# Kernel optimization log

Measured on AMD Instinct MI355X. Metric: run time of the kernel, lower is better.

## Reference

```python
import jax, jax.numpy as jnp
import numpy as np

B, T_CTX, N_EMBD, N_ATTN, N_HEAD = 8, 1024, 1024, 1024, 16
HEAD_SIZE = N_ATTN // N_HEAD


def _init_time_w():
    # replicates the torch init: per-head exponential decay curves
    curve = np.array([-(T_CTX - 1 - i) for i in range(T_CTX)], dtype=np.float64)
    ww = np.ones((N_HEAD, T_CTX), dtype=np.float32)
    for h in range(N_HEAD):
        if h < N_HEAD - 1:
            decay_speed = T_CTX ** (-(h + 1) / (N_HEAD - 1))
        else:
            decay_speed = 0.0
        ww[h] = np.exp(curve * decay_speed).astype(np.float32)
    return jnp.asarray(ww)


def setup_inputs() -> dict:
    key = jax.random.key(0)
    ks = jax.random.split(key, 6)
    s = 0.02
    return {
        "x": jax.random.normal(ks[0], (B, T_CTX, N_EMBD), jnp.float32),
        "time_w": _init_time_w(),                                   # [H, TT]
        "time_alpha": jnp.ones((N_HEAD, 1, T_CTX), jnp.float32),
        "time_beta": jnp.ones((N_HEAD, T_CTX, 1), jnp.float32),
        "time_gamma": jnp.ones((T_CTX, 1), jnp.float32),
        "Wk": jax.random.normal(ks[1], (N_ATTN, N_EMBD), jnp.float32) * s,
        "bk": jnp.zeros((N_ATTN,), jnp.float32),
        "Wv": jax.random.normal(ks[2], (N_ATTN, N_EMBD), jnp.float32) * s,
        "bv": jnp.zeros((N_ATTN,), jnp.float32),
        "Wr": jax.random.normal(ks[3], (N_ATTN, N_EMBD), jnp.float32) * s,
        "br": jnp.zeros((N_ATTN,), jnp.float32),
        "Wo": jax.random.normal(ks[4], (N_EMBD, N_ATTN), jnp.float32) * s,
        "bo": jnp.zeros((N_EMBD,), jnp.float32),
    }


def _build_w(time_w, time_alpha, time_beta, T):
    # w[h,t,u] = time_w[h, TT-1-(t-u)] for u<=t else 0  (causal decay matrix)
    TT = time_w.shape[1]
    t = jnp.arange(T)[:, None]
    u = jnp.arange(T)[None, :]
    idx = jnp.clip((TT - 1) - t + u, 0, TT - 1)
    mask = u <= t
    w = jnp.where(mask[None, :, :], time_w[:, idx], 0.0)  # [H, T, T]
    return w * time_alpha[:, :, :T] * time_beta[:, :T, :]


def reference(x, time_w, time_alpha, time_beta, time_gamma,
              Wk, bk, Wv, bv, Wr, br, Wo, bo):
    Bb, T, C = x.shape
    H = time_w.shape[0]
    w = _build_w(time_w, time_alpha, time_beta, T)  # [H,T,T]

    # time shift on the first half of channels: prepend zero row, drop last
    x_half = jnp.pad(x[:, :, : C // 2], ((0, 0), (1, 0), (0, 0)))[:, :T, :]
    xs = jnp.concatenate([x_half, x[:, :, C // 2 :]], axis=-1)

    k = xs @ Wk.T + bk
    v = xs @ Wv.T + bv
    r = xs @ Wr.T + br

    k = jnp.exp(jnp.clip(k, -60.0, 30.0))
    sum_k = jnp.cumsum(k, axis=1)  # [B,T,NA]

    kv = (k * v).reshape(Bb, T, H, -1)               # [B,T,H,hs]
    wkv = jnp.einsum('htu,buhc->bthc', w, kv).reshape(Bb, T, -1)

    rwkv = jax.nn.sigmoid(r) * wkv / sum_k
    out = rwkv @ Wo.T + bo
    return out * time_gamma[:T]
```

## Files before the change

### kernel.cpp

```cpp
#include <hip/hip_runtime.h>
#include <hip/hip_bf16.h>
#include <cstddef>
#include <cstdint>

#define B_SZ   8
#define T_CTX  1024
#define C_DIM  1024
#define H_NUM  16
#define HS     64
#define M_ROWS (B_SZ * T_CTX)

typedef __attribute__((ext_vector_type(8))) short bf16x8;
typedef __attribute__((ext_vector_type(8))) unsigned short u16x8;
typedef __attribute__((ext_vector_type(4))) float f32x4;

static __device__ inline unsigned short f2bf(float f) {
    __hip_bfloat16 h = __float2bfloat16(f);
    return __builtin_bit_cast(unsigned short, h);
}
static __device__ inline float bf2f(unsigned short u) {
    unsigned int v = ((unsigned int)u) << 16;
    return __builtin_bit_cast(float, v);
}
static __device__ inline void gld16(const void* g, void* l) {
    __builtin_amdgcn_global_load_lds((const __attribute__((address_space(1))) void*)g,
                                     (__attribute__((address_space(3))) void*)l,
                                     16, 0, 0);
}

__global__ __launch_bounds__(256)
void convert_all(const float* __restrict__ x, unsigned short* __restrict__ xs,
                 const float* __restrict__ Wk, const float* __restrict__ Wv,
                 const float* __restrict__ Wr, const float* __restrict__ Wo,
                 unsigned short* __restrict__ wdst)
{
    const int bid = blockIdx.x;
    if (bid < 8192) {
        const int idx = (bid * 256 + threadIdx.x) * 4;
        const int m = idx >> 10;
        const int c = idx & 1023;
        float4 v;
        if (c < 512) {
            const int t = m & (T_CTX - 1);
            if (t == 0) v = make_float4(0.f, 0.f, 0.f, 0.f);
            else        v = *(const float4*)(x + (size_t)(m - 1) * C_DIM + c);
        } else {
            v = *(const float4*)(x + idx);
        }
        ushort4 o;
        o.x = f2bf(v.x); o.y = f2bf(v.y); o.z = f2bf(v.z); o.w = f2bf(v.w);
        *(ushort4*)(xs + idx) = o;
    } else {
        const int wid = bid - 8192;
        const int z = wid >> 10;
        const float* src = (z == 0) ? Wk : (z == 1) ? Wv : (z == 2) ? Wr : Wo;
        const int idx = ((wid & 1023) * 256 + threadIdx.x) * 4;
        const float4 v = *(const float4*)(src + idx);
        ushort4 o;
        o.x = f2bf(v.x); o.y = f2bf(v.y); o.z = f2bf(v.z); o.w = f2bf(v.w);
        *(ushort4*)(wdst + (size_t)z * (C_DIM * C_DIM) + idx) = o;
    }
}

__global__ __launch_bounds__(256, 2)
void mfma_gemm64(const unsigned short* __restrict__ A,
                 const unsigned short* __restrict__ Wb,
                 const float* __restrict__ b0, const float* __restrict__ b1,
                 const float* __restrict__ b2,
                 void* __restrict__ o0, void* __restrict__ o1, void* __restrict__ o2,
                 const float* __restrict__ gamma, int multi)
{
    const int d  = blockIdx.x;
    const int y  = ((d & 7) << 3) | ((d >> 3) & 7);
    const int xb = d >> 6;
    const int m0 = y * 128, n0 = xb * 128;

    int mode, ncol0;
    const float* bias;
    void* out;
    if (multi) {
        const int z = n0 >> 10;
        mode = z;
        ncol0 = n0 & 1023;
        bias = (z == 0) ? b0 : (z == 1) ? b1 : b2;
        out  = (z == 0) ? o0 : (z == 1) ? o1 : o2;
    } else {
        mode = 3; ncol0 = n0; bias = b0; out = o0;
    }

    __shared__ unsigned short Sh[2 * 128 * 64];

    const int tid = threadIdx.x;
    const int w = tid >> 6, l = tid & 63;

    const int r8  = l >> 3;
    const int c16 = ((l & 7) ^ r8) * 8;
    const unsigned short* gA = A  + (size_t)(m0 + w * 32 + r8) * C_DIM + c16;
    const unsigned short* gB = Wb + (size_t)(n0 + w * 32 + r8) * C_DIM + c16;
    char* lA = (char*)Sh + (w * 32) * 128;
    char* lB = (char*)Sh + 16384 + (w * 32) * 128;

    const int wr = w >> 1, wc = w & 1;
    const int lr = l & 15, lkq = l >> 4;
    const int x7 = lr & 7;

    f32x4 acc[4][4];
    #pragma unroll
    for (int i = 0; i < 4; ++i)
        #pragma unroll
        for (int j = 0; j < 4; ++j) acc[i][j] = (f32x4){0.f, 0.f, 0.f, 0.f};

    for (int k0 = 0; k0 < C_DIM; k0 += 64) {
        #pragma unroll
        for (int r = 0; r < 4; ++r) {
            gld16(gA + k0 + (size_t)r * 8 * C_DIM, lA + r * 8 * 128);
            gld16(gB + k0 + (size_t)r * 8 * C_DIM, lB + r * 8 * 128);
        }
        __syncthreads();

        bf16x8 af[2][4], bfv[2][4];
        #pragma unroll
        for (int ks = 0; ks < 2; ++ks) {
            const int slot = ((ks * 4 + lkq) ^ x7) * 8;
            #pragma unroll
            for (int i = 0; i < 4; ++i)
                af[ks][i] = *(const bf16x8*)&Sh[(wr * 64 + i * 16 + lr) * 64 + slot];
            #pragma unroll
            for (int j = 0; j < 4; ++j)
                bfv[ks][j] = *(const bf16x8*)&Sh[8192 + (wc * 64 + j * 16 + lr) * 64 + slot];
        }
        #pragma unroll
        for (int ks = 0; ks < 2; ++ks)
            #pragma unroll
            for (int i = 0; i < 4; ++i)
                #pragma unroll
                for (int j = 0; j < 4; ++j)
                    acc[i][j] = __builtin_amdgcn_mfma_f32_16x16x32_bf16(
                        af[ks][i], bfv[ks][j], acc[i][j], 0, 0, 0);
        __syncthreads();
    }

    if (mode == 1 || mode == 2) {
        char* const Cs = (char*)Sh;
        #pragma unroll
        for (int j = 0; j < 4; ++j) {
            const int col_l = wc * 64 + j * 16 + lr;
            const float bz = bias[ncol0 + col_l];
            #pragma unroll
            for (int i = 0; i < 4; ++i) {
                const int rbl = wr * 64 + i * 16 + lkq * 4;
                #pragma unroll
                for (int r = 0; r < 4; ++r) {
                    const int row_l = rbl + r;
                    float v = acc[i][j][r] + bz;
                    if (mode == 2) v = 1.f / (1.f + __expf(-v));
                    const int byte = row_l * 256 + ((col_l * 2) ^ (((row_l >> 2) & 7) << 5));
                    *(unsigned short*)(Cs + byte) = f2bf(v);
                }
            }
        }
        __syncthreads();
        #pragma unroll
        for (int it = 0; it < 8; ++it) {
            const int row_l = (tid >> 4) + it * 16;
            const int k = tid & 15;
            const int byte = row_l * 256 + ((k * 16) ^ (((row_l >> 2) & 7) << 5));
            const u16x8 v = *(const u16x8*)(Cs + byte);
            *(u16x8*)((unsigned short*)out + (size_t)(m0 + row_l) * C_DIM + ncol0 + k * 8) = v;
        }
    } else {
        #pragma unroll
        for (int j = 0; j < 4; ++j) {
            const int col = ncol0 + wc * 64 + j * 16 + lr;
            const float bz = bias[col];
            #pragma unroll
            for (int i = 0; i < 4; ++i) {
                const int rb = m0 + wr * 64 + i * 16 + lkq * 4;
                #pragma unroll
                for (int r = 0; r < 4; ++r) {
                    const int row = rb + r;
                    float v = acc[i][j][r] + bz;
                    if (mode == 0)      v = __expf(fminf(fmaxf(v, -60.f), 30.f));
                    else                v *= gamma[row & (T_CTX - 1)];
                    ((float*)out)[(size_t)row * C_DIM + col] = v;
                }
            }
        }
    }
}

__global__ __launch_bounds__(256)
void cumsum_chunk(const float* __restrict__ expk, const unsigned short* __restrict__ vbf,
                  const float* __restrict__ alpha,
                  float* __restrict__ sumk, unsigned short* __restrict__ kvT,
                  float* __restrict__ aux)
{
    __shared__ unsigned short kvs[4][64 * 68];
    const int tid = threadIdx.x;
    const int w = tid >> 6, l = tid & 63;
    const int n = blockIdx.x * 256 + tid;
    const int q = blockIdx.y;
    const int b = blockIdx.z;
    const int h = n >> 6;
    const size_t base = ((size_t)b * T_CTX + q * 64) * C_DIM + n;
    const float* arow = alpha + h * T_CTX + q * 64;

    float s = 0.f;
    for (int g = 0; g < 8; ++g) {
        u16x8 buf;
        #pragma unroll
        for (int k = 0; k < 8; ++k) {
            const int i = g * 8 + k;
            const size_t idx = base + (size_t)i * C_DIM;
            const float e  = expk[idx];
            const float vv = bf2f(vbf[idx]);
            s += e;
            sumk[idx] = s;
            buf[k] = f2bf(e * vv * arow[i]);
        }
        *(u16x8*)&kvs[w][l * 68 + g * 8] = buf;
    }
    aux[((size_t)b * 16 + q) * C_DIM + n] = s;

    __syncthreads();

    const int u8 = (l & 7) * 8;
    #pragma unroll
    for (int r = 0; r < 8; ++r) {
        const int c2 = (l >> 3) + r * 8;
        const u16x8 v = *(const u16x8*)&kvs[w][c2 * 68 + u8];
        *(u16x8*)(kvT + (((size_t)b * H_NUM + h) * HS + c2) * T_CTX + q * 64 + u8) = v;
    }
}

#define REPL_STRIDE 1176
#define REPL_USED   1168

__global__ __launch_bounds__(256)
void wkv_mfma(const unsigned short* __restrict__ kvT,
              const float* __restrict__ sumk,
              const unsigned short* __restrict__ sigr,
              const float* __restrict__ tw, const float* __restrict__ beta,
              const float* __restrict__ aux,
              unsigned short* __restrict__ rwkv)
{
    __shared__ unsigned short repl[8 * REPL_STRIDE];
    __shared__ unsigned short kv_s[64 * 72];
    __shared__ unsigned short tw_s[1024];
    __shared__ unsigned short cst[128 * 64];

    const int tid = threadIdx.x;
    const int bxp = blockIdx.x;
    const int h  = blockIdx.y;
    const int b  = blockIdx.z;

    {
        const int i = tid * 4;
        const float4 v = *(const float4*)(tw + h * T_CTX + i);
        ushort4 o;
        o.x = f2bf(v.x); o.y = f2bf(v.y); o.z = f2bf(v.z); o.w = f2bf(v.w);
        *(ushort4*)&tw_s[i] = o;
    }
    __syncthreads();

    #pragma unroll
    for (int r = 0; r < 8; ++r)
        for (int i = tid; i < REPL_USED; i += 256) {
            const int src = i + r;
            repl[r * REPL_STRIDE + i] = (src < 1024) ? tw_s[src] : (unsigned short)0;
        }

    const int w = tid >> 6, l = tid & 63;
    const int wr = w >> 1, wc = w & 1;
    const int lr = l & 15, lkq = l >> 4;
    const int r    = (7 - lr) & 7;
    const char* repl_c = (const char*)repl;

    const int srow = tid >> 2;
    const int ucol = (tid & 3) * 16;
    const unsigned short* gkv = kvT + (((size_t)b * H_NUM + h) * HS + srow) * T_CTX + ucol;
    unsigned short* skv = &kv_s[srow * 72 + ucol];

    for (int pass = 0; pass < 2; ++pass) {
        const int bx = pass ? (7 - bxp) : bxp;
        const int t0 = bx * 128;
        const int S0 = 1023 - t0 - wr * 64 - lr + lkq * 8;
        const int abase = 2 * S0 + (2 * REPL_STRIDE - 2) * r;

        f32x4 acc[4][2];
        #pragma unroll
        for (int i = 0; i < 4; ++i) {
            acc[i][0] = (f32x4){0.f, 0.f, 0.f, 0.f};
            acc[i][1] = (f32x4){0.f, 0.f, 0.f, 0.f};
        }

        const int nsteps = t0 / 64 + 2;
        u16x8 q0 = *(const u16x8*)(gkv);
        u16x8 q1 = *(const u16x8*)(gkv + 8);
        for (int ks = 0; ks < nsteps; ++ks) {
            __syncthreads();
            *(u16x8*)skv       = q0;
            *(u16x8*)(skv + 8) = q1;
            __syncthreads();
            if (ks + 1 < nsteps) {
                const int un = (ks + 1) * 64;
                q0 = *(const u16x8*)(gkv + un);
                q1 = *(const u16x8*)(gkv + un + 8);
            }

            const int ub = abase + 2 * (ks * 64);
            #pragma unroll
            for (int kk = 0; kk < 2; ++kk) {
                bf16x8 af[4], bfv[2];
                #pragma unroll
                for (int i = 0; i < 4; ++i)
                    af[i] = *(const bf16x8*)(repl_c + (ub + kk * 64 - i * 32));
                #pragma unroll
                for (int j = 0; j < 2; ++j)
                    bfv[j] = *(const bf16x8*)&kv_s[(wc * 32 + j * 16 + lr) * 72 + kk * 32 + lkq * 8];
                #pragma unroll
                for (int i = 0; i < 4; ++i)
                    #pragma unroll
                    for (int j = 0; j < 2; ++j)
                        acc[i][j] = __builtin_amdgcn_mfma_f32_16x16x32_bf16(
                            af[i], bfv[j], acc[i][j], 0, 0, 0);
            }
        }

        const int cq = 2 * bx + wr;
        float off[2];
        #pragma unroll
        for (int j = 0; j < 2; ++j) {
            const int cl = wc * 32 + j * 16 + lr;
            float o = 0.f;
            for (int q = 0; q < cq; ++q)
                o += aux[((size_t)b * 16 + q) * C_DIM + h * HS + cl];
            off[j] = o;
        }

        char* const Cc = (char*)cst;
        #pragma unroll
        for (int i = 0; i < 4; ++i) {
            const int rbl = wr * 64 + i * 16 + lkq * 4;
            #pragma unroll
            for (int rg = 0; rg < 4; ++rg) {
                const int row_l = rbl + rg;
                const int t = t0 + row_l;
                const float bet = beta[h * T_CTX + t];
                const size_t row_off = ((size_t)(b * T_CTX + t)) * C_DIM + h * HS;
                #pragma unroll
                for (int j = 0; j < 2; ++j) {
                    const int cl = wc * 32 + j * 16 + lr;
                    const float sk = sumk[row_off + cl] + off[j];
                    const float sr = bf2f(sigr[row_off + cl]);
                    const int byte = row_l * 128 + ((cl * 2) ^ (((row_l >> 2) & 3) << 5));
                    *(unsigned short*)(Cc + byte) = f2bf(sr * bet * acc[i][j][rg] / sk);
                }
            }
        }
        __syncthreads();
        #pragma unroll
        for (int it = 0; it < 4; ++it) {
            const int row_l = (tid >> 3) + it * 32;
            const int k = tid & 7;
            const int byte = row_l * 128 + ((k * 16) ^ (((row_l >> 2) & 3) << 5));
            const u16x8 v = *(const u16x8*)(Cc + byte);
            *(u16x8*)(rwkv + ((size_t)(b * T_CTX + t0 + row_l)) * C_DIM + h * HS + k * 8) = v;
        }
        __syncthreads();
    }
}

extern "C" void kernel_launch(void* const* d_in, const int* in_sizes, int n_in,
                              void* d_out, int out_size, void* d_ws, size_t ws_size,
                              hipStream_t stream)
{
    const float* x     = (const float*)d_in[0];
    const float* tw    = (const float*)d_in[1];
    const float* alpha = (const float*)d_in[2];
    const float* beta  = (const float*)d_in[3];
    const float* gamma = (const float*)d_in[4];
    const float* Wk    = (const float*)d_in[5];
    const float* bk    = (const float*)d_in[6];
    const float* Wv    = (const float*)d_in[7];
    const float* bv    = (const float*)d_in[8];
    const float* Wr    = (const float*)d_in[9];
    const float* br    = (const float*)d_in[10];
    const float* Wo    = (const float*)d_in[11];
    const float* bo    = (const float*)d_in[12];
    float* out = (float*)d_out;

    char* W = (char*)d_ws;
    float* expk          = (float*)W;
    unsigned short* rwkv = (unsigned short*)W;
    unsigned short* vbf  = (unsigned short*)(W + (32ull << 20));
    unsigned short* wbf  = (unsigned short*)(W + (48ull << 20));
    float* aux           = (float*)(W + (56ull << 20));
    float* sumk          = (float*)(W + (64ull << 20));
    unsigned short* xs   = (unsigned short*)(W + (64ull << 20));
    unsigned short* sigr = (unsigned short*)(W + (96ull << 20));
    unsigned short* kvT  = (unsigned short*)(W + (112ull << 20));

    const size_t WSZ = (size_t)C_DIM * C_DIM;

    convert_all<<<dim3(12288), 256, 0, stream>>>(x, xs, Wk, Wv, Wr, Wo, wbf);

    mfma_gemm64<<<dim3(1536), 256, 0, stream>>>(
        xs, wbf, bk, bv, br, expk, vbf, sigr, gamma, 1);

    cumsum_chunk<<<dim3(4, 16, 8), 256, 0, stream>>>(expk, vbf, alpha, sumk, kvT, aux);

    wkv_mfma<<<dim3(4, 16, 8), 256, 0, stream>>>(
        kvT, sumk, sigr, tw, beta, aux, rwkv);

    mfma_gemm64<<<dim3(512), 256, 0, stream>>>(
        rwkv, wbf + 3 * WSZ, bo, nullptr, nullptr,
        out, nullptr, nullptr, gamma, 0);
}
```

Before: 252.5 us.

## Double-buffer kv tiles in WKV kernel, remap grid, hoist aux offsets

The WKV MFMA kernel now keeps two LDS buffers for the kv tile. The next tile's global load and LDS store overlap with the current tile's MFMAs, which leaves one barrier per step instead of two. The launch becomes a 1D grid with a custom block-to-(pass,head,batch) mapping, likely for better L2 locality or load balance. The aux prefix-offset reduction for both passes is hoisted before the main loop. The cost is extra LDS (another 64x72 bf16 tile), which may lower occupancy.

```diff
diff --git a/kernel.cpp b/kernel.cpp
--- a/kernel.cpp
+++ b/kernel.cpp
@@ -245,14 +245,16 @@
               unsigned short* __restrict__ rwkv)
 {
     __shared__ unsigned short repl[8 * REPL_STRIDE];
-    __shared__ unsigned short kv_s[64 * 72];
+    __shared__ unsigned short kv_s[2][64 * 72];
     __shared__ unsigned short tw_s[1024];
     __shared__ unsigned short cst[128 * 64];
 
     const int tid = threadIdx.x;
-    const int bxp = blockIdx.x;
-    const int h  = blockIdx.y;
-    const int b  = blockIdx.z;
+    const int id  = blockIdx.x;
+    const int bxp = (id >> 3) & 3;
+    const int g   = (id & 7) | ((id >> 5) << 3);
+    const int h   = g & 15;
+    const int b   = g >> 4;
 
     {
         const int i = tid * 4;
@@ -279,7 +281,21 @@
     const int srow = tid >> 2;
     const int ucol = (tid & 3) * 16;
     const unsigned short* gkv = kvT + (((size_t)b * H_NUM + h) * HS + srow) * T_CTX + ucol;
-    unsigned short* skv = &kv_s[srow * 72 + ucol];
+
+    float off01[2][2];
+    #pragma unroll
+    for (int p = 0; p < 2; ++p) {
+        const int bx = p ? (7 - bxp) : bxp;
+        const int cq = 2 * bx + wr;
+        #pragma unroll
+        for (int j = 0; j < 2; ++j) {
+            const int cl = wc * 32 + j * 16 + lr;
+            float o = 0.f;
+            for (int q = 0; q < cq; ++q)
+                o += aux[((size_t)b * 16 + q) * C_DIM + h * HS + cl];
+            off01[p][j] = o;
+        }
+    }
 
     for (int pass = 0; pass < 2; ++pass) {
         const int bx = pass ? (7 - bxp) : bxp;
@@ -295,19 +311,27 @@
         }
 
         const int nsteps = t0 / 64 + 2;
-        u16x8 q0 = *(const u16x8*)(gkv);
-        u16x8 q1 = *(const u16x8*)(gkv + 8);
+
+        {
+            const u16x8 p0 = *(const u16x8*)(gkv);
+            const u16x8 p1 = *(const u16x8*)(gkv + 8);
+            unsigned short* skv = &kv_s[0][srow * 72 + ucol];
+            *(u16x8*)skv       = p0;
+            *(u16x8*)(skv + 8) = p1;
+        }
+        __syncthreads();
+
+        int cur = 0;
         for (int ks = 0; ks < nsteps; ++ks) {
-            __syncthreads();
-            *(u16x8*)skv       = q0;
-            *(u16x8*)(skv + 8) = q1;
-            __syncthreads();
-            if (ks + 1 < nsteps) {
+            u16x8 qn0, qn1;
+            const bool more = (ks + 1 < nsteps);
+            if (more) {
                 const int un = (ks + 1) * 64;
-                q0 = *(const u16x8*)(gkv + un);
-                q1 = *(const u16x8*)(gkv + un + 8);
-            }
-
+                qn0 = *(const u16x8*)(gkv + un);
+                qn1 = *(const u16x8*)(gkv + un + 8);
+            }
+
+            const unsigned short* kcur = &kv_s[cur][0];
             const int ub = abase + 2 * (ks * 64);
             #pragma unroll
             for (int kk = 0; kk < 2; ++kk) {
@@ -317,7 +341,7 @@
                     af[i] = *(const bf16x8*)(repl_c + (ub + kk * 64 - i * 32));
                 #pragma unroll
                 for (int j = 0; j < 2; ++j)
-                    bfv[j] = *(const bf16x8*)&kv_s[(wc * 32 + j * 16 + lr) * 72 + kk * 32 + lkq * 8];
+                    bfv[j] = *(const bf16x8*)&kcur[(wc * 32 + j * 16 + lr) * 72 + kk * 32 + lkq * 8];
                 #pragma unroll
                 for (int i = 0; i < 4; ++i)
                     #pragma unroll
@@ -325,17 +349,14 @@
                         acc[i][j] = __builtin_amdgcn_mfma_f32_16x16x32_bf16(
                             af[i], bfv[j], acc[i][j], 0, 0, 0);
             }
-        }
-
-        const int cq = 2 * bx + wr;
-        float off[2];
-        #pragma unroll
-        for (int j = 0; j < 2; ++j) {
-            const int cl = wc * 32 + j * 16 + lr;
-            float o = 0.f;
-            for (int q = 0; q < cq; ++q)
-                o += aux[((size_t)b * 16 + q) * C_DIM + h * HS + cl];
-            off[j] = o;
+
+            if (more) {
+                unsigned short* skv = &kv_s[cur ^ 1][srow * 72 + ucol];
+                *(u16x8*)skv       = qn0;
+                *(u16x8*)(skv + 8) = qn1;
+            }
+            __syncthreads();
+            cur ^= 1;
         }
 
         char* const Cc = (char*)cst;
@@ -351,7 +372,7 @@
                 #pragma unroll
                 for (int j = 0; j < 2; ++j) {
                     const int cl = wc * 32 + j * 16 + lr;
-                    const float sk = sumk[row_off + cl] + off[j];
+                    const float sk = sumk[row_off + cl] + off01[pass][j];
                     const float sr = bf2f(sigr[row_off + cl]);
                     const int byte = row_l * 128 + ((cl * 2) ^ (((row_l >> 2) & 3) << 5));
                     *(unsigned short*)(Cc + byte) = f2bf(sr * bet * acc[i][j][rg] / sk);
@@ -410,7 +431,7 @@
 
     cumsum_chunk<<<dim3(4, 16, 8), 256, 0, stream>>>(expk, vbf, alpha, sumk, kvT, aux);
 
-    wkv_mfma<<<dim3(4, 16, 8), 256, 0, stream>>>(
+    wkv_mfma<<<dim3(512), 256, 0, stream>>>(
         kvT, sumk, sigr, tw, beta, aux, rwkv);
 
     mfma_gemm64<<<dim3(512), 256, 0, stream>>>(
```

After: 260.2 us. 3.0% more time.
